# Optimization experiments

Measured on AMD Instinct MI355X. Metric: run time of the kernel, lower is better.

The kernel has to match this reference:

```python
import jax, jax.numpy as jnp
import numpy as np

MIN_NORM = 1e-15
BALL_EPS = 4e-3  # float32 boundary eps used by HGCN PoincareBall


def _norm(x):
    return jnp.clip(jnp.linalg.norm(x, axis=-1, keepdims=True), MIN_NORM, None)


def _artanh(x):
    x = jnp.clip(x, -1.0 + 1e-7, 1.0 - 1e-7)
    return 0.5 * (jnp.log1p(x) - jnp.log1p(-x))


def proj(x, c):
    n = _norm(x)
    maxnorm = (1.0 - BALL_EPS) / jnp.sqrt(c)
    return jnp.where(n > maxnorm, x / n * maxnorm, x)


def expmap0(u, c):
    sc = jnp.sqrt(c)
    n = _norm(u)
    return jnp.tanh(sc * n) * u / (sc * n)


def logmap0(p, c):
    sc = jnp.sqrt(c)
    n = _norm(p)
    return _artanh(sc * n) * p / (sc * n)


def mobius_matvec(W, x, c):
    sc = jnp.sqrt(c)
    xn = _norm(x)
    mx = x @ W.T
    mxn = _norm(mx)
    res = jnp.tanh(mxn / xn * _artanh(sc * xn)) * mx / (mxn * sc)
    cond = jnp.all(mx == 0, axis=-1, keepdims=True)
    return jnp.where(cond, jnp.zeros((), x.dtype), res)


def mobius_add(x, y, c):
    x2 = jnp.sum(x * x, axis=-1, keepdims=True)
    y2 = jnp.sum(y * y, axis=-1, keepdims=True)
    xy = jnp.sum(x * y, axis=-1, keepdims=True)
    num = (1.0 + 2.0 * c * xy + c * y2) * x + (1.0 - c * x2) * y
    den = 1.0 + 2.0 * c * xy + c * c * x2 * y2
    return num / jnp.clip(den, MIN_NORM, None)


N, D_IN, D_OUT, E = 50000, 128, 128, 600000
C_IN, C_OUT = 1.0, 1.0


def setup_inputs() -> dict:
    key = jax.random.key(0)
    k1, k2, k3, k4, k5, k6 = jax.random.split(key, 6)
    x = jax.random.normal(k1, (N, D_IN), dtype=jnp.float32) * 1e-3  # points near ball origin
    x = proj(x, C_IN)
    W = jax.random.normal(k2, (D_OUT, D_IN), dtype=jnp.float32) * (1.0 / np.sqrt(D_IN))
    b = jax.random.normal(k3, (D_OUT,), dtype=jnp.float32) * 1e-3
    edge_w = jax.random.uniform(k4, (E,), dtype=jnp.float32)
    src = jax.random.randint(k5, (E,), 0, N, dtype=jnp.int32)
    dst = jax.random.randint(k6, (E,), 0, N, dtype=jnp.int32)
    return {"x": x, "W": W, "b": b, "edge_w": edge_w, "src": src, "dst": dst}


def reference(x, W, b, edge_w, src, dst):
    # HypLinear (inference: no dropout on weight)
    h = proj(mobius_matvec(W, x, C_IN), C_IN)
    hyp_bias = proj(expmap0(b[None, :], C_IN), C_IN)  # proj_tan0 is identity
    h = proj(mobius_add(h, hyp_bias, C_IN), C_IN)
    # HypAgg (use_att=0): logmap0 -> spmm -> expmap0 -> proj
    xt = logmap0(h, C_IN)                               # [N, D]
    msgs = edge_w[:, None] * xt[src]                    # [E, D] gather
    agg = jax.ops.segment_sum(msgs, dst, num_segments=N)
    h = proj(expmap0(agg, C_IN), C_IN)
    # HypAct: relu in tangent space, re-map with c_out
    t = jax.nn.relu(logmap0(h, C_IN))
    out = proj(expmap0(t, C_OUT), C_OUT)
    return out
```

## Files before the change

### kernel.cpp

```cpp
#include <hip/hip_runtime.h>
#include <math.h>

#define MAXNORM 0.996f
#define MAXDEG 64

typedef _Float16 h2 __attribute__((ext_vector_type(2)));
typedef _Float16 h8v __attribute__((ext_vector_type(8)));
typedef float f4v __attribute__((ext_vector_type(4)));

__device__ __forceinline__ float wave_sum(float v) {
#pragma unroll
  for (int off = 32; off > 0; off >>= 1) v += __shfl_xor(v, off, 64);
  return v;
}

__device__ __forceinline__ float fast_tanh(float x) {
  float e = __expf(2.0f * x);
  return (e - 1.0f) * __builtin_amdgcn_rcpf(e + 1.0f);
}

__device__ __forceinline__ float fast_artanh(float x) {
  x = fminf(x, 1.0f - 1e-7f);
  return 0.5f * __logf((1.0f + x) * __builtin_amdgcn_rcpf(1.0f - x));
}

__device__ __forceinline__ void proj2(float& v0, float& v1) {
  float n = fmaxf(sqrtf(wave_sum(v0 * v0 + v1 * v1)), 1e-15f);
  if (n > MAXNORM) {
    float s = MAXNORM / n;
    v0 *= s;
    v1 *= s;
  }
}

__global__ void k_fill(int* __restrict__ p, int n4) {
  int i = blockIdx.x * blockDim.x + threadIdx.x;
  if (i < n4) ((int4*)p)[i] = make_int4(0, 0, 0, 0);
}

__global__ __launch_bounds__(256, 4) void k_lin_scatter(
    const float* __restrict__ x, const float* __restrict__ W,
    const float* __restrict__ b, const int* __restrict__ src,
    const int* __restrict__ dst, const float* __restrict__ ew,
    int* __restrict__ deg, unsigned* __restrict__ csr,
    _Float16* __restrict__ xt, int N, int E, int nbLin) {
  if ((int)blockIdx.x >= nbLin) {
    int id = blockIdx.x - nbLin;
    int stride = (gridDim.x - nbLin) * 256;
    for (int e = id * 256 + threadIdx.x; e < E; e += stride) {
      int d = dst[e];
      int t = atomicAdd(&deg[d], 1);
      if (t < MAXDEG) {
        unsigned wq = (unsigned)fmaf(ew[e], 65535.0f, 0.5f);
        csr[((size_t)d << 6) + t] = (unsigned)src[e] | (wq << 16);
      }
    }
    return;
  }

  __shared__ _Float16 WsH[128 * 128];
  __shared__ float biasLds[132];
  const int t = threadIdx.x;
  const int lane = t & 63;
  const int wv = t >> 6;

  const float4* W4 = (const float4*)W;
#pragma unroll
  for (int i = 0; i < 16; ++i) {
    int f = t + 256 * i;
    int o = f >> 5;
    int k4 = (f & 31) << 2;
    float4 v = W4[f];
    unsigned lo = __builtin_bit_cast(unsigned, __builtin_amdgcn_cvt_pkrtz(v.x, v.y));
    unsigned hi = __builtin_bit_cast(unsigned, __builtin_amdgcn_cvt_pkrtz(v.z, v.w));
    *(uint2*)&WsH[o * 128 + (k4 ^ ((o & 7) << 3))] = make_uint2(lo, hi);
  }

  if (t < 64) {
    float b0 = b[t], b1 = b[t + 64];
    float nb = fmaxf(sqrtf(wave_sum(b0 * b0 + b1 * b1)), 1e-15f);
    float s = fast_tanh(nb) * __builtin_amdgcn_rcpf(nb);
    float h0 = b0 * s, h1 = b1 * s;
    proj2(h0, h1);
    float y2w = wave_sum(h0 * h0 + h1 * h1);
    biasLds[t] = h0;
    biasLds[t + 64] = h1;
    if (t == 0) biasLds[128] = y2w;
  }
  __syncthreads();

  const int col = lane & 15;
  const int g = lane >> 4;
  float hbv[8];
#pragma unroll
  for (int n = 0; n < 8; ++n) hbv[n] = biasLds[col + 16 * n];
  const float y2 = biasLds[128];
  const float4* X4 = (const float4*)x;
  const int osw = (col & 7) << 3;

  for (int half = 0; half < 2; ++half) {
    const int stripe0 = blockIdx.x * 128 + half * 64 + wv * 16;
    int arow = stripe0 + col;
    if (arow >= N) arow = N - 1;

    h8v af[4];
    float pxr = 0.f;
#pragma unroll
    for (int s = 0; s < 4; ++s) {
      float4 a = X4[(size_t)arow * 32 + 8 * s + 2 * g];
      float4 c = X4[(size_t)arow * 32 + 8 * s + 2 * g + 1];
      pxr = fmaf(a.x, a.x, pxr);
      pxr = fmaf(a.y, a.y, pxr);
      pxr = fmaf(a.z, a.z, pxr);
      pxr = fmaf(a.w, a.w, pxr);
      pxr = fmaf(c.x, c.x, pxr);
      pxr = fmaf(c.y, c.y, pxr);
      pxr = fmaf(c.z, c.z, pxr);
      pxr = fmaf(c.w, c.w, pxr);
      union {
        uint4 u;
        h8v h;
      } cv;
      cv.u = make_uint4(
          __builtin_bit_cast(unsigned, __builtin_amdgcn_cvt_pkrtz(a.x, a.y)),
          __builtin_bit_cast(unsigned, __builtin_amdgcn_cvt_pkrtz(a.z, a.w)),
          __builtin_bit_cast(unsigned, __builtin_amdgcn_cvt_pkrtz(c.x, c.y)),
          __builtin_bit_cast(unsigned, __builtin_amdgcn_cvt_pkrtz(c.z, c.w)));
      af[s] = cv.h;
    }
    pxr += __shfl_xor(pxr, 16, 64);
    pxr += __shfl_xor(pxr, 32, 64);

    f4v acc[8];
    const f4v zero = {0.f, 0.f, 0.f, 0.f};
#pragma unroll
    for (int n = 0; n < 8; ++n) acc[n] = zero;

#pragma unroll
    for (int n = 0; n < 8; ++n) {
      const int obase = (16 * n + col) * 128;
#pragma unroll
      for (int s = 0; s < 4; ++s) {
        h8v bf = *(const h8v*)&WsH[obase + ((32 * s + 8 * g) ^ osw)];
        acc[n] = __builtin_amdgcn_mfma_f32_16x16x32_f16(af[s], bf, acc[n], 0, 0, 0);
      }
    }

#pragma unroll
    for (int r = 0; r < 4; ++r) {
      float pm = 0.f, pxy = 0.f;
#pragma unroll
      for (int n = 0; n < 8; ++n) {
        float v = acc[n][r];
        pm = fmaf(v, v, pm);
        pxy = fmaf(v, hbv[n], pxy);
      }
#pragma unroll
      for (int off = 1; off < 16; off <<= 1) {
        pm += __shfl_xor(pm, off, 64);
        pxy += __shfl_xor(pxy, off, 64);
      }
      const int irow = g * 4 + r;
      float px = __shfl(pxr, irow, 64);
      float xn = fmaxf(sqrtf(px), 1e-15f);
      float mxn = fmaxf(sqrtf(pm), 1e-15f);
      float s1 = fast_tanh(mxn * __builtin_amdgcn_rcpf(xn) * fast_artanh(xn)) *
                 __builtin_amdgcn_rcpf(mxn);
      if (pm == 0.0f) s1 = 0.0f;
      float nv = s1 * mxn;
      if (nv > MAXNORM) {
        s1 *= MAXNORM / nv;
        nv = MAXNORM;
      }
      float x2 = nv * nv;
      float xy = s1 * pxy;
      float A = 1.0f + 2.0f * xy + y2;
      float B = 1.0f - x2;
      float den = fmaxf(1.0f + 2.0f * xy + x2 * y2, 1e-15f);
      float rden = __builtin_amdgcn_rcpf(den);
      float rn2 = fmaxf(A * A * x2 + 2.0f * A * B * xy + B * B * y2, 0.0f);
      float rn = sqrtf(rn2) * rden;
      float gs = 1.0f;
      if (rn > MAXNORM) gs = MAXNORM / rn;
      float ng = fmaxf(fminf(rn, MAXNORM), 1e-15f);
      float slog = fast_artanh(ng) * __builtin_amdgcn_rcpf(ng);
      float ftot = slog * gs * rden;
      float f1 = ftot * A * s1;
      float f2 = ftot * B;
      const int growm = stripe0 + irow;
      if (growm < N) {
        _Float16* dp = xt + (size_t)growm * 128 + col;
#pragma unroll
        for (int n = 0; n < 8; ++n) dp[16 * n] = (_Float16)(f1 * acc[n][r] + f2 * hbv[n]);
      }
    }
  }
}

__global__ __launch_bounds__(256) void k_agg_final(
    const _Float16* __restrict__ xt, const unsigned* __restrict__ csr,
    const int* __restrict__ deg, float* __restrict__ out, int N) {
  int n0 = blockIdx.x * 4 + (threadIdx.x >> 6);
  const int lane = threadIdx.x & 63;
  if (n0 >= N) return;
  const int n = __builtin_amdgcn_readfirstlane(n0);
  int dg = deg[n];
  if (dg > MAXDEG) dg = MAXDEG;
  const unsigned* row = csr + ((size_t)n << 6);
  float a0 = 0.f, a1 = 0.f;
  const float wsc = 1.0f / 65535.0f;
  for (int e = 0; e < dg; e += 16) {
    unsigned c[16];
#pragma unroll
    for (int i = 0; i < 16; ++i) c[i] = row[e + i];
    h2 u[16];
#pragma unroll
    for (int i = 0; i < 16; ++i) {
      int idx = (int)(c[i] & 0xFFFFu);
      if (idx > N - 1) idx = N - 1;
      const h2* r = (const h2*)xt + ((size_t)idx << 6);
      u[i] = r[lane];
    }
#pragma unroll
    for (int i = 0; i < 16; ++i) {
      float w = (e + i < dg) ? (float)(c[i] >> 16) * wsc : 0.0f;
      a0 = fmaf(w, (float)u[i][0], a0);
      a1 = fmaf(w, (float)u[i][1], a1);
    }
  }

  float p0 = fmaxf(a0, 0.0f), p1 = fmaxf(a1, 0.0f);
  float an2 = a0 * a0 + a1 * a1;
  float pos2 = p0 * p0 + p1 * p1;
#pragma unroll
  for (int off = 32; off > 0; off >>= 1) {
    an2 += __shfl_xor(an2, off, 64);
    pos2 += __shfl_xor(pos2, off, 64);
  }
  float an = fmaxf(sqrtf(an2), 1e-15f);
  float th = fast_tanh(an);
  float fh = th * __builtin_amdgcn_rcpf(an);
  float hn = th;
  if (th > MAXNORM) {
    fh = MAXNORM * __builtin_amdgcn_rcpf(an);
    hn = MAXNORM;
  }
  float hn_c = fmaxf(hn, 1e-15f);
  float c1 = fh * fast_artanh(hn_c) * __builtin_amdgcn_rcpf(hn_c);
  float tn = fmaxf(c1 * sqrtf(pos2), 1e-15f);
  float ts = fast_tanh(tn);
  float s2 = ts * __builtin_amdgcn_rcpf(tn);
  float gs = 1.0f;
  if (ts > MAXNORM) gs = MAXNORM * __builtin_amdgcn_rcpf(ts);
  float f = s2 * gs * c1;
  ((float2*)(out + (size_t)n * 128))[lane] = make_float2(f * p0, f * p1);
}

__global__ void k_edge(const h2* __restrict__ xt, const float* __restrict__ ew,
                       const int* __restrict__ src, const int* __restrict__ dst,
                       float* __restrict__ agg, int E) {
  int tid = blockIdx.x * blockDim.x + threadIdx.x;
  int gw = tid >> 6;
  int lane = tid & 63;
  int nw = (gridDim.x * blockDim.x) >> 6;
  for (int e = gw; e < E; e += nw) {
    int s = src[e];
    int d = dst[e];
    float wgt = ew[e];
    h2 v = xt[(size_t)s * 64 + lane];
    float* base = agg + (size_t)d * 128 + 2 * lane;
    unsafeAtomicAdd(base, (float)v[0] * wgt);
    unsafeAtomicAdd(base + 1, (float)v[1] * wgt);
  }
}

__global__ void k_final(const float* __restrict__ agg, float* __restrict__ out, int N) {
  int gw = blockIdx.x * 4 + (threadIdx.x >> 6);
  int lane = threadIdx.x & 63;
  if (gw >= N) return;
  float2 v = ((const float2*)(agg + (size_t)gw * 128))[lane];
  float a0 = v.x, a1 = v.y;
  float p0 = fmaxf(a0, 0.0f), p1 = fmaxf(a1, 0.0f);
  float an2 = a0 * a0 + a1 * a1;
  float pos2 = p0 * p0 + p1 * p1;
#pragma unroll
  for (int off = 32; off > 0; off >>= 1) {
    an2 += __shfl_xor(an2, off, 64);
    pos2 += __shfl_xor(pos2, off, 64);
  }
  float an = fmaxf(sqrtf(an2), 1e-15f);
  float th = fast_tanh(an);
  float fh = th * __builtin_amdgcn_rcpf(an);
  float hn = th;
  if (th > MAXNORM) {
    fh = MAXNORM * __builtin_amdgcn_rcpf(an);
    hn = MAXNORM;
  }
  float hn_c = fmaxf(hn, 1e-15f);
  float c1 = fh * fast_artanh(hn_c) * __builtin_amdgcn_rcpf(hn_c);
  float tn = fmaxf(c1 * sqrtf(pos2), 1e-15f);
  float ts = fast_tanh(tn);
  float s2 = ts * __builtin_amdgcn_rcpf(tn);
  float gs = 1.0f;
  if (ts > MAXNORM) gs = MAXNORM * __builtin_amdgcn_rcpf(ts);
  float f = s2 * gs * c1;
  ((float2*)(out + (size_t)gw * 128))[lane] = make_float2(f * p0, f * p1);
}

static inline size_t pad256(size_t x) { return (x + 255) & ~(size_t)255; }

extern "C" void kernel_launch(void* const* d_in, const int* in_sizes, int n_in,
                              void* d_out, int out_size, void* d_ws, size_t ws_size,
                              hipStream_t stream) {
  const float* x = (const float*)d_in[0];
  const float* W = (const float*)d_in[1];
  const float* b = (const float*)d_in[2];
  const float* ew = (const float*)d_in[3];
  const int* src = (const int*)d_in[4];
  const int* dst = (const int*)d_in[5];
  float* out = (float*)d_out;
  const int N = in_sizes[0] / 128;
  const int E = in_sizes[3];

  char* p = (char*)d_ws;
  int* deg = (int*)p;           p += pad256((size_t)N * 4);
  unsigned* csr = (unsigned*)p; p += pad256((size_t)N * MAXDEG * 4);
  _Float16* xt = (_Float16*)p;  p += (size_t)N * 256;
  size_t need = (size_t)(p - (char*)d_ws);

  const int nbLin = (N + 127) / 128;
  if (ws_size >= need && N <= 65536) {
    const int n4 = (N + 3) / 4;
    k_fill<<<(n4 + 255) / 256, 256, 0, stream>>>(deg, n4);
    int nbScat = 1024 - (nbLin % 1024);
    if (nbScat < 256) nbScat += 1024;
    k_lin_scatter<<<nbLin + nbScat, 256, 0, stream>>>(x, W, b, src, dst, ew, deg, csr,
                                                      xt, N, E, nbLin);
    k_agg_final<<<(N + 3) / 4, 256, 0, stream>>>(xt, csr, deg, out, N);
  } else {
    float* agg = (float*)d_ws;
    _Float16* xth = (_Float16*)d_out;
    (void)hipMemsetAsync(agg, 0, (size_t)N * 128 * sizeof(float), stream);
    k_lin_scatter<<<nbLin, 256, 0, stream>>>(x, W, b, nullptr, nullptr, nullptr,
                                             nullptr, nullptr, xth, N, 0, nbLin);
    k_edge<<<2048, 256, 0, stream>>>((const h2*)xth, ew, src, dst, agg, E);
    k_final<<<(N + 3) / 4, 256, 0, stream>>>(agg, out, N);
  }
}
```

Before: 88.11 us.

## Pre-convert W to fp16 in prep kernel, drop LDS staging, flatten scatter grid

The degree zeroing is fused with a one-time fp16 conversion of W into workspace. The fused linear/scatter kernel no longer stages W in shared memory and instead reads fp16 W fragments straight from global or L2. It computes the bias per wave with shuffles, processes 64 rows per block instead of 128, and uses one edge per thread with no grid-stride loop. This removes per-block LDS fill, barrier and occupancy limits, but each wave now issues redundant global loads of W. The fallback path moves to a separate LDS-based linear kernel.

```diff
diff --git a/kernel.cpp b/kernel.cpp
--- a/kernel.cpp
+++ b/kernel.cpp
@@ -33,21 +33,29 @@
   }
 }
 
-__global__ void k_fill(int* __restrict__ p, int n4) {
-  int i = blockIdx.x * blockDim.x + threadIdx.x;
-  if (i < n4) ((int4*)p)[i] = make_int4(0, 0, 0, 0);
-}
-
-__global__ __launch_bounds__(256, 4) void k_lin_scatter(
-    const float* __restrict__ x, const float* __restrict__ W,
+__global__ void k_prep(int* __restrict__ deg, int n4, int nf,
+                       const float* __restrict__ W, _Float16* __restrict__ wh) {
+  if ((int)blockIdx.x < nf) {
+    int i = blockIdx.x * 256 + threadIdx.x;
+    if (i < n4) ((int4*)deg)[i] = make_int4(0, 0, 0, 0);
+  } else {
+    int j = (blockIdx.x - nf) * 256 + threadIdx.x;
+    float4 v = ((const float4*)W)[j];
+    unsigned lo = __builtin_bit_cast(unsigned, __builtin_amdgcn_cvt_pkrtz(v.x, v.y));
+    unsigned hi = __builtin_bit_cast(unsigned, __builtin_amdgcn_cvt_pkrtz(v.z, v.w));
+    ((uint2*)wh)[j] = make_uint2(lo, hi);
+  }
+}
+
+__global__ __launch_bounds__(256) void k_lin_scatter(
+    const float* __restrict__ x, const _Float16* __restrict__ wh,
     const float* __restrict__ b, const int* __restrict__ src,
     const int* __restrict__ dst, const float* __restrict__ ew,
     int* __restrict__ deg, unsigned* __restrict__ csr,
     _Float16* __restrict__ xt, int N, int E, int nbLin) {
   if ((int)blockIdx.x >= nbLin) {
-    int id = blockIdx.x - nbLin;
-    int stride = (gridDim.x - nbLin) * 256;
-    for (int e = id * 256 + threadIdx.x; e < E; e += stride) {
+    int e = (blockIdx.x - nbLin) * 256 + threadIdx.x;
+    if (e < E) {
       int d = dst[e];
       int t = atomicAdd(&deg[d], 1);
       if (t < MAXDEG) {
@@ -58,141 +66,122 @@
     return;
   }
 
-  __shared__ _Float16 WsH[128 * 128];
-  __shared__ float biasLds[132];
   const int t = threadIdx.x;
   const int lane = t & 63;
   const int wv = t >> 6;
-
-  const float4* W4 = (const float4*)W;
-#pragma unroll
-  for (int i = 0; i < 16; ++i) {
-    int f = t + 256 * i;
-    int o = f >> 5;
-    int k4 = (f & 31) << 2;
-    float4 v = W4[f];
-    unsigned lo = __builtin_bit_cast(unsigned, __builtin_amdgcn_cvt_pkrtz(v.x, v.y));
-    unsigned hi = __builtin_bit_cast(unsigned, __builtin_amdgcn_cvt_pkrtz(v.z, v.w));
-    *(uint2*)&WsH[o * 128 + (k4 ^ ((o & 7) << 3))] = make_uint2(lo, hi);
-  }
-
-  if (t < 64) {
-    float b0 = b[t], b1 = b[t + 64];
+  const int col = lane & 15;
+  const int g = lane >> 4;
+
+  float hb0, hb1, y2;
+  {
+    float b0 = b[lane], b1 = b[lane + 64];
     float nb = fmaxf(sqrtf(wave_sum(b0 * b0 + b1 * b1)), 1e-15f);
     float s = fast_tanh(nb) * __builtin_amdgcn_rcpf(nb);
-    float h0 = b0 * s, h1 = b1 * s;
-    proj2(h0, h1);
-    float y2w = wave_sum(h0 * h0 + h1 * h1);
-    biasLds[t] = h0;
-    biasLds[t + 64] = h1;
-    if (t == 0) biasLds[128] = y2w;
-  }
-  __syncthreads();
-
-  const int col = lane & 15;
-  const int g = lane >> 4;
+    hb0 = b0 * s;
+    hb1 = b1 * s;
+    proj2(hb0, hb1);
+    y2 = wave_sum(hb0 * hb0 + hb1 * hb1);
+  }
   float hbv[8];
 #pragma unroll
-  for (int n = 0; n < 8; ++n) hbv[n] = biasLds[col + 16 * n];
-  const float y2 = biasLds[128];
+  for (int n = 0; n < 4; ++n) hbv[n] = __shfl(hb0, col + 16 * n, 64);
+#pragma unroll
+  for (int n = 4; n < 8; ++n) hbv[n] = __shfl(hb1, col + 16 * (n - 4), 64);
+
+  const int stripe0 = blockIdx.x * 64 + wv * 16;
+  int arow = stripe0 + col;
+  if (arow >= N) arow = N - 1;
   const float4* X4 = (const float4*)x;
-  const int osw = (col & 7) << 3;
-
-  for (int half = 0; half < 2; ++half) {
-    const int stripe0 = blockIdx.x * 128 + half * 64 + wv * 16;
-    int arow = stripe0 + col;
-    if (arow >= N) arow = N - 1;
-
-    h8v af[4];
-    float pxr = 0.f;
+
+  h8v af[4];
+  float pxr = 0.f;
+#pragma unroll
+  for (int s = 0; s < 4; ++s) {
+    float4 a = X4[(size_t)arow * 32 + 8 * s + 2 * g];
+    float4 c = X4[(size_t)arow * 32 + 8 * s + 2 * g + 1];
+    pxr = fmaf(a.x, a.x, pxr);
+    pxr = fmaf(a.y, a.y, pxr);
+    pxr = fmaf(a.z, a.z, pxr);
+    pxr = fmaf(a.w, a.w, pxr);
+    pxr = fmaf(c.x, c.x, pxr);
+    pxr = fmaf(c.y, c.y, pxr);
+    pxr = fmaf(c.z, c.z, pxr);
+    pxr = fmaf(c.w, c.w, pxr);
+    union {
+      uint4 u;
+      h8v h;
+    } cv;
+    cv.u = make_uint4(
+        __builtin_bit_cast(unsigned, __builtin_amdgcn_cvt_pkrtz(a.x, a.y)),
+        __builtin_bit_cast(unsigned, __builtin_amdgcn_cvt_pkrtz(a.z, a.w)),
+        __builtin_bit_cast(unsigned, __builtin_amdgcn_cvt_pkrtz(c.x, c.y)),
+        __builtin_bit_cast(unsigned, __builtin_amdgcn_cvt_pkrtz(c.z, c.w)));
+    af[s] = cv.h;
+  }
+  pxr += __shfl_xor(pxr, 16, 64);
+  pxr += __shfl_xor(pxr, 32, 64);
+
+  f4v acc[8];
+  const f4v zero = {0.f, 0.f, 0.f, 0.f};
+#pragma unroll
+  for (int n = 0; n < 8; ++n) acc[n] = zero;
+
+#pragma unroll
+  for (int n = 0; n < 8; ++n) {
+    const int obase = (16 * n + col) * 128;
 #pragma unroll
     for (int s = 0; s < 4; ++s) {
-      float4 a = X4[(size_t)arow * 32 + 8 * s + 2 * g];
-      float4 c = X4[(size_t)arow * 32 + 8 * s + 2 * g + 1];
-      pxr = fmaf(a.x, a.x, pxr);
-      pxr = fmaf(a.y, a.y, pxr);
-      pxr = fmaf(a.z, a.z, pxr);
-      pxr = fmaf(a.w, a.w, pxr);
-      pxr = fmaf(c.x, c.x, pxr);
-      pxr = fmaf(c.y, c.y, pxr);
-      pxr = fmaf(c.z, c.z, pxr);
-      pxr = fmaf(c.w, c.w, pxr);
-      union {
-        uint4 u;
-        h8v h;
-      } cv;
-      cv.u = make_uint4(
-          __builtin_bit_cast(unsigned, __builtin_amdgcn_cvt_pkrtz(a.x, a.y)),
-          __builtin_bit_cast(unsigned, __builtin_amdgcn_cvt_pkrtz(a.z, a.w)),
-          __builtin_bit_cast(unsigned, __builtin_amdgcn_cvt_pkrtz(c.x, c.y)),
-          __builtin_bit_cast(unsigned, __builtin_amdgcn_cvt_pkrtz(c.z, c.w)));
-      af[s] = cv.h;
-    }
-    pxr += __shfl_xor(pxr, 16, 64);
-    pxr += __shfl_xor(pxr, 32, 64);
-
-    f4v acc[8];
-    const f4v zero = {0.f, 0.f, 0.f, 0.f};
-#pragma unroll
-    for (int n = 0; n < 8; ++n) acc[n] = zero;
-
+      h8v bf = *(const h8v*)&wh[obase + 32 * s + 8 * g];
+      acc[n] = __builtin_amdgcn_mfma_f32_16x16x32_f16(af[s], bf, acc[n], 0, 0, 0);
+    }
+  }
+
+#pragma unroll
+  for (int r = 0; r < 4; ++r) {
+    float pm = 0.f, pxy = 0.f;
 #pragma unroll
     for (int n = 0; n < 8; ++n) {
-      const int obase = (16 * n + col) * 128;
-#pragma unroll
-      for (int s = 0; s < 4; ++s) {
-        h8v bf = *(const h8v*)&WsH[obase + ((32 * s + 8 * g) ^ osw)];
-        acc[n] = __builtin_amdgcn_mfma_f32_16x16x32_f16(af[s], bf, acc[n], 0, 0, 0);
-      }
-    }
-
-#pragma unroll
-    for (int r = 0; r < 4; ++r) {
-      float pm = 0.f, pxy = 0.f;
-#pragma unroll
-      for (int n = 0; n < 8; ++n) {
-        float v = acc[n][r];
-        pm = fmaf(v, v, pm);
-        pxy = fmaf(v, hbv[n], pxy);
-      }
-#pragma unroll
-      for (int off = 1; off < 16; off <<= 1) {
-        pm += __shfl_xor(pm, off, 64);
-        pxy += __shfl_xor(pxy, off, 64);
-      }
-      const int irow = g * 4 + r;
-      float px = __shfl(pxr, irow, 64);
-      float xn = fmaxf(sqrtf(px), 1e-15f);
-      float mxn = fmaxf(sqrtf(pm), 1e-15f);
-      float s1 = fast_tanh(mxn * __builtin_amdgcn_rcpf(xn) * fast_artanh(xn)) *
-                 __builtin_amdgcn_rcpf(mxn);
-      if (pm == 0.0f) s1 = 0.0f;
-      float nv = s1 * mxn;
-      if (nv > MAXNORM) {
-        s1 *= MAXNORM / nv;
-        nv = MAXNORM;
-      }
-      float x2 = nv * nv;
-      float xy = s1 * pxy;
-      float A = 1.0f + 2.0f * xy + y2;
-      float B = 1.0f - x2;
-      float den = fmaxf(1.0f + 2.0f * xy + x2 * y2, 1e-15f);
-      float rden = __builtin_amdgcn_rcpf(den);
-      float rn2 = fmaxf(A * A * x2 + 2.0f * A * B * xy + B * B * y2, 0.0f);
-      float rn = sqrtf(rn2) * rden;
-      float gs = 1.0f;
-      if (rn > MAXNORM) gs = MAXNORM / rn;
-      float ng = fmaxf(fminf(rn, MAXNORM), 1e-15f);
-      float slog = fast_artanh(ng) * __builtin_amdgcn_rcpf(ng);
-      float ftot = slog * gs * rden;
-      float f1 = ftot * A * s1;
-      float f2 = ftot * B;
-      const int growm = stripe0 + irow;
-      if (growm < N) {
-        _Float16* dp = xt + (size_t)growm * 128 + col;
-#pragma unroll
-        for (int n = 0; n < 8; ++n) dp[16 * n] = (_Float16)(f1 * acc[n][r] + f2 * hbv[n]);
-      }
+      float v = acc[n][r];
+      pm = fmaf(v, v, pm);
+      pxy = fmaf(v, hbv[n], pxy);
+    }
+#pragma unroll
+    for (int off = 1; off < 16; off <<= 1) {
+      pm += __shfl_xor(pm, off, 64);
+      pxy += __shfl_xor(pxy, off, 64);
+    }
+    const int irow = g * 4 + r;
+    float px = __shfl(pxr, irow, 64);
+    float xn = fmaxf(sqrtf(px), 1e-15f);
+    float mxn = fmaxf(sqrtf(pm), 1e-15f);
+    float s1 = fast_tanh(mxn * __builtin_amdgcn_rcpf(xn) * fast_artanh(xn)) *
+               __builtin_amdgcn_rcpf(mxn);
+    if (pm == 0.0f) s1 = 0.0f;
+    float nv = s1 * mxn;
+    if (nv > MAXNORM) {
+      s1 *= MAXNORM / nv;
+      nv = MAXNORM;
+    }
+    float x2 = nv * nv;
+    float xy = s1 * pxy;
+    float A = 1.0f + 2.0f * xy + y2;
+    float B = 1.0f - x2;
+    float den = fmaxf(1.0f + 2.0f * xy + x2 * y2, 1e-15f);
+    float rden = __builtin_amdgcn_rcpf(den);
+    float rn2 = fmaxf(A * A * x2 + 2.0f * A * B * xy + B * B * y2, 0.0f);
+    float rn = sqrtf(rn2) * rden;
+    float gs = 1.0f;
+    if (rn > MAXNORM) gs = MAXNORM / rn;
+    float ng = fmaxf(fminf(rn, MAXNORM), 1e-15f);
+    float slog = fast_artanh(ng) * __builtin_amdgcn_rcpf(ng);
+    float ftot = slog * gs * rden;
+    float f1 = ftot * A * s1;
+    float f2 = ftot * B;
+    const int growm = stripe0 + irow;
+    if (growm < N) {
+      _Float16* dp = xt + (size_t)growm * 128 + col;
+#pragma unroll
+      for (int n = 0; n < 8; ++n) dp[16 * n] = (_Float16)(f1 * acc[n][r] + f2 * hbv[n]);
     }
   }
 }
@@ -254,6 +243,138 @@
   if (ts > MAXNORM) gs = MAXNORM * __builtin_amdgcn_rcpf(ts);
   float f = s2 * gs * c1;
   ((float2*)(out + (size_t)n * 128))[lane] = make_float2(f * p0, f * p1);
+}
+
+__global__ __launch_bounds__(256, 4) void k_linear_lds(
+    const float* __restrict__ x, const float* __restrict__ W,
+    const float* __restrict__ b, _Float16* __restrict__ xt, int N) {
+  __shared__ _Float16 WsH[128 * 128];
+  __shared__ float biasLds[132];
+  const int t = threadIdx.x;
+  const int lane = t & 63;
+  const int wv = t >> 6;
+  const float4* W4 = (const float4*)W;
+#pragma unroll
+  for (int i = 0; i < 16; ++i) {
+    int f = t + 256 * i;
+    int o = f >> 5;
+    int k4 = (f & 31) << 2;
+    float4 v = W4[f];
+    unsigned lo = __builtin_bit_cast(unsigned, __builtin_amdgcn_cvt_pkrtz(v.x, v.y));
+    unsigned hi = __builtin_bit_cast(unsigned, __builtin_amdgcn_cvt_pkrtz(v.z, v.w));
+    *(uint2*)&WsH[o * 128 + (k4 ^ ((o & 7) << 3))] = make_uint2(lo, hi);
+  }
+  if (t < 64) {
+    float b0 = b[t], b1 = b[t + 64];
+    float nb = fmaxf(sqrtf(wave_sum(b0 * b0 + b1 * b1)), 1e-15f);
+    float s = fast_tanh(nb) * __builtin_amdgcn_rcpf(nb);
+    float h0 = b0 * s, h1 = b1 * s;
+    proj2(h0, h1);
+    float y2w = wave_sum(h0 * h0 + h1 * h1);
+    biasLds[t] = h0;
+    biasLds[t + 64] = h1;
+    if (t == 0) biasLds[128] = y2w;
+  }
+  __syncthreads();
+  const int col = lane & 15;
+  const int g = lane >> 4;
+  float hbv[8];
+#pragma unroll
+  for (int n = 0; n < 8; ++n) hbv[n] = biasLds[col + 16 * n];
+  const float y2 = biasLds[128];
+  const float4* X4 = (const float4*)x;
+  const int osw = (col & 7) << 3;
+  const int stripe0 = blockIdx.x * 64 + wv * 16;
+  int arow = stripe0 + col;
+  if (arow >= N) arow = N - 1;
+  h8v af[4];
+  float pxr = 0.f;
+#pragma unroll
+  for (int s = 0; s < 4; ++s) {
+    float4 a = X4[(size_t)arow * 32 + 8 * s + 2 * g];
+    float4 c = X4[(size_t)arow * 32 + 8 * s + 2 * g + 1];
+    pxr = fmaf(a.x, a.x, pxr);
+    pxr = fmaf(a.y, a.y, pxr);
+    pxr = fmaf(a.z, a.z, pxr);
+    pxr = fmaf(a.w, a.w, pxr);
+    pxr = fmaf(c.x, c.x, pxr);
+    pxr = fmaf(c.y, c.y, pxr);
+    pxr = fmaf(c.z, c.z, pxr);
+    pxr = fmaf(c.w, c.w, pxr);
+    union {
+      uint4 u;
+      h8v h;
+    } cv;
+    cv.u = make_uint4(
+        __builtin_bit_cast(unsigned, __builtin_amdgcn_cvt_pkrtz(a.x, a.y)),
+        __builtin_bit_cast(unsigned, __builtin_amdgcn_cvt_pkrtz(a.z, a.w)),
+        __builtin_bit_cast(unsigned, __builtin_amdgcn_cvt_pkrtz(c.x, c.y)),
+        __builtin_bit_cast(unsigned, __builtin_amdgcn_cvt_pkrtz(c.z, c.w)));
+    af[s] = cv.h;
+  }
+  pxr += __shfl_xor(pxr, 16, 64);
+  pxr += __shfl_xor(pxr, 32, 64);
+  f4v acc[8];
+  const f4v zero = {0.f, 0.f, 0.f, 0.f};
+#pragma unroll
+  for (int n = 0; n < 8; ++n) acc[n] = zero;
+#pragma unroll
+  for (int n = 0; n < 8; ++n) {
+    const int obase = (16 * n + col) * 128;
+#pragma unroll
+    for (int s = 0; s < 4; ++s) {
+      h8v bf = *(const h8v*)&WsH[obase + ((32 * s + 8 * g) ^ osw)];
+      acc[n] = __builtin_amdgcn_mfma_f32_16x16x32_f16(af[s], bf, acc[n], 0, 0, 0);
+    }
+  }
+#pragma unroll
+  for (int r = 0; r < 4; ++r) {
+    float pm = 0.f, pxy = 0.f;
+#pragma unroll
+    for (int n = 0; n < 8; ++n) {
+      float v = acc[n][r];
+      pm = fmaf(v, v, pm);
+      pxy = fmaf(v, hbv[n], pxy);
+    }
+#pragma unroll
+    for (int off = 1; off < 16; off <<= 1) {
+      pm += __shfl_xor(pm, off, 64);
+      pxy += __shfl_xor(pxy, off, 64);
+    }
+    const int irow = g * 4 + r;
+    float px = __shfl(pxr, irow, 64);
+    float xn = fmaxf(sqrtf(px), 1e-15f);
+    float mxn = fmaxf(sqrtf(pm), 1e-15f);
+    float s1 = fast_tanh(mxn * __builtin_amdgcn_rcpf(xn) * fast_artanh(xn)) *
+               __builtin_amdgcn_rcpf(mxn);
+    if (pm == 0.0f) s1 = 0.0f;
+    float nv = s1 * mxn;
+    if (nv > MAXNORM) {
+      s1 *= MAXNORM / nv;
+      nv = MAXNORM;
+    }
+    float x2 = nv * nv;
+    float xy = s1 * pxy;
+    float A = 1.0f + 2.0f * xy + y2;
+    float B = 1.0f - x2;
+    float den = fmaxf(1.0f + 2.0f * xy + x2 * y2, 1e-15f);
+    float rden = __builtin_amdgcn_rcpf(den);
+    float rn2 = fmaxf(A * A * x2 + 2.0f * A * B * xy + B * B * y2, 0.0f);
+    float rn = sqrtf(rn2) * rden;
+    float gs = 1.0f;
+    if (rn > MAXNORM) gs = MAXNORM / rn;
+    float ng = fmaxf(fminf(rn, MAXNORM), 1e-15f);
+    float slog = fast_artanh(ng) * __builtin_amdgcn_rcpf(ng);
+    float ftot = slog * gs * rden;
+    float f1 = ftot * A * s1;
+    float f2 = ftot * B;
+    const int growm = stripe0 + irow;
+    if (growm < N) {
+      _Float16* dp = xt + (size_t)growm * 128 + col;
+#pragma unroll
+      for (int n = 0; n < 8; ++n) dp[16 * n] = (_Float16)(f1 * acc[n][r] + f2 * hbv[n]);
+    }
+  }
 }
 
 __global__ void k_edge(const h2* __restrict__ xt, const float* __restrict__ ew,
@@ -326,23 +447,23 @@
   int* deg = (int*)p;           p += pad256((size_t)N * 4);
   unsigned* csr = (unsigned*)p; p += pad256((size_t)N * MAXDEG * 4);
   _Float16* xt = (_Float16*)p;  p += (size_t)N * 256;
+  _Float16* wh = (_Float16*)p;  p += 128 * 128 * 2;
   size_t need = (size_t)(p - (char*)d_ws);
 
-  const int nbLin = (N + 127) / 128;
   if (ws_size >= need && N <= 65536) {
     const int n4 = (N + 3) / 4;
-    k_fill<<<(n4 + 255) / 256, 256, 0, stream>>>(deg, n4);
-    int nbScat = 1024 - (nbLin % 1024);
-    if (nbScat < 256) nbScat += 1024;
-    k_lin_scatter<<<nbLin + nbScat, 256, 0, stream>>>(x, W, b, src, dst, ew, deg, csr,
+    const int nf = (n4 + 255) / 256;
+    k_prep<<<nf + 16, 256, 0, stream>>>(deg, n4, nf, W, wh);
+    const int nbLin = (N + 63) / 64;
+    const int nbScat = (E + 255) / 256;
+    k_lin_scatter<<<nbLin + nbScat, 256, 0, stream>>>(x, wh, b, src, dst, ew, deg, csr,
                                                       xt, N, E, nbLin);
     k_agg_final<<<(N + 3) / 4, 256, 0, stream>>>(xt, csr, deg, out, N);
   } else {
     float* agg = (float*)d_ws;
     _Float16* xth = (_Float16*)d_out;
     (void)hipMemsetAsync(agg, 0, (size_t)N * 128 * sizeof(float), stream);
-    k_lin_scatter<<<nbLin, 256, 0, stream>>>(x, W, b, nullptr, nullptr, nullptr,
-                                             nullptr, nullptr, xth, N, 0, nbLin);
+    k_linear_lds<<<(N + 63) / 64, 256, 0, stream>>>(x, W, b, xth, N);
     k_edge<<<2048, 256, 0, stream>>>((const h2*)xth, ew, src, dst, agg, E);
     k_final<<<(N + 3) / 4, 256, 0, stream>>>(agg, out, N);
   }
```

Result: slower. 93.33 us (+5.9%).
